# Kernel optimization log

Hardware: AMD Instinct MI355X
Metric: run time of the kernel (lower is better)

## Reference

```python
import jax, jax.numpy as jnp
import numpy as np

B, T, N, E = 4, 32, 370, 11840
H, HEADS, DH, L, K = 64, 4, 16, 3, 5

def gelu(x):
    return jax.nn.gelu(x, approximate=False)  # torch default GELU is exact erf

def setup_inputs() -> dict:
    key = jax.random.key(0)
    ks = jax.random.split(key, 18)
    s = 0.05  # keep activations well-scaled
    return {
        "x": jax.random.normal(ks[0], (B, T, N, H), jnp.float32),
        "edge_index": jax.random.randint(ks[1], (2, E), 0, N, dtype=jnp.int32),
        "edge_weight": jax.random.uniform(ks[2], (E,), jnp.float32),
        "W_gcn": jax.random.normal(ks[3], (L, H, H), jnp.float32) * s,
        "b_gcn": jax.random.normal(ks[4], (L, H), jnp.float32) * s,
        "W_gat": jax.random.normal(ks[5], (L, H, HEADS * DH), jnp.float32) * s,
        "att_src": jax.random.normal(ks[6], (L, HEADS, DH), jnp.float32) * s,
        "att_dst": jax.random.normal(ks[7], (L, HEADS, DH), jnp.float32) * s,
        "b_gat": jax.random.normal(ks[8], (L, HEADS * DH), jnp.float32) * s,
        "W_t": jax.random.normal(ks[9], (L, H, H, K), jnp.float32) * s,  # (O,I,K)
        "b_t": jax.random.normal(ks[10], (L, H), jnp.float32) * s,
        "ln_g": jnp.ones((L, H), jnp.float32),
        "ln_b": jnp.zeros((L, H), jnp.float32),
        "W1": jax.random.normal(ks[11], (N * H, 256), jnp.float32) * s,
        "b1": jax.random.normal(ks[12], (256,), jnp.float32) * s,
        "W2": jax.random.normal(ks[13], (256, 64), jnp.float32) * s,
        "b2": jax.random.normal(ks[14], (64,), jnp.float32) * s,
    }

def reference(x, edge_index, edge_weight, W_gcn, b_gcn, W_gat, att_src, att_dst,
              b_gat, W_t, b_t, ln_g, ln_b, W1, b1, W2, b2):
    Bb, Tt, Nn, Ff = x.shape
    G = Bb * Tt
    nL = W_gcn.shape[0]
    heads, dh = att_src.shape[1], att_src.shape[2]
    Hh = heads * dh
    # shared topology across all G graphs; add self-loops (PyG default, fill=1.0)
    src, dst = edge_index[0], edge_index[1]
    loop = jnp.arange(Nn, dtype=src.dtype)
    src2 = jnp.concatenate([src, loop])
    dst2 = jnp.concatenate([dst, loop])
    ew2 = jnp.concatenate([edge_weight, jnp.ones((Nn,), edge_weight.dtype)])
    # symmetric GCN normalization (same for every graph in the batch)
    deg = jnp.zeros((Nn,), x.dtype).at[dst2].add(ew2)
    dis = jnp.where(deg > 0, jax.lax.rsqrt(deg), jnp.zeros_like(deg))
    gnorm = dis[src2] * ew2 * dis[dst2]                       # (E2,)
    h = x.reshape(G, Nn, Ff)
    for l in range(nL):
        # ---- GCNConv: transform -> gather -> weighted scatter-add ----
        hw = h @ W_gcn[l]                                     # (G,N,H)
        msg = hw[:, src2] * gnorm[None, :, None]              # (G,E2,H)
        g = jnp.zeros_like(hw).at[:, dst2].add(msg) + b_gcn[l]
        g = gelu(g)
        # ---- GATConv: per-edge softmax attention over incoming edges ----
        gh = (g @ W_gat[l]).reshape(G, Nn, heads, dh)
        asrc = (gh * att_src[l]).sum(-1)                      # (G,N,heads)
        adst = (gh * att_dst[l]).sum(-1)
        e = jax.nn.leaky_relu(asrc[:, src2] + adst[:, dst2], negative_slope=0.2)
        m = jnp.full((G, Nn, heads), -jnp.inf, e.dtype).at[:, dst2].max(e)
        ex = jnp.exp(e - m[:, dst2])
        den = jnp.zeros((G, Nn, heads), e.dtype).at[:, dst2].add(ex)
        alpha = ex / den[:, dst2]                             # (G,E2,heads)
        msgs = gh[:, src2] * alpha[..., None]                 # (G,E2,heads,dh)
        out = jnp.zeros_like(gh).at[:, dst2].add(msgs).reshape(G, Nn, Hh) + b_gat[l]
        # ---- residual + LayerNorm ----
        r = out + h[..., :Hh]
        mu = r.mean(-1, keepdims=True)
        var = ((r - mu) ** 2).mean(-1, keepdims=True)
        h = (r - mu) * jax.lax.rsqrt(var + 1e-5) * ln_g[l] + ln_b[l]
    # ---- temporal convs over T per (batch, node) ----
    Hc = h.shape[-1]
    xt = h.reshape(Bb, Tt, Nn, Hc).transpose(0, 2, 3, 1).reshape(Bb * Nn, Hc, Tt)
    for l in range(nL):
        c = jax.lax.conv_general_dilated(
            xt, W_t[l], (1,), "SAME", dimension_numbers=("NCH", "OIH", "NCH"))
        xt = gelu(c + b_t[l][None, :, None]) + xt
    z = xt.reshape(Bb, Nn, Hc, Tt).transpose(0, 3, 1, 2).reshape(Bb, Tt, Nn * Hc)
    return gelu(z @ W1 + b1) @ W2 + b2
```

## Files before the change

kernel.cpp:

```cpp
#include <hip/hip_runtime.h>
#include <hip/hip_bf16.h>

#define B_   4
#define T_   32
#define N_   370
#define NP_  384
#define E_   11840
#define E2_  12210
#define H_   64
#define G_   128
#define GN_  47360
#define BN_  1480
#define NH_  23680
#define ECAP 320
#define KCH_ 128
#define NCH_ 185

typedef __hip_bfloat16 bf;
typedef short short8 __attribute__((ext_vector_type(8)));
typedef float f32x4 __attribute__((ext_vector_type(4)));

__device__ __forceinline__ float gelu_f(float x){
  return 0.5f * x * (1.0f + erff(x * 0.7071067811865475f));
}
__device__ __forceinline__ float lrelu(float v){ return v > 0.f ? v : 0.2f * v; }
__device__ __forceinline__ float b2f(bf x){ return __bfloat162float(x); }
__device__ __forceinline__ void store_bf4(bf* p, float4 v){
  bf tmp[4] = {__float2bfloat16(v.x), __float2bfloat16(v.y),
               __float2bfloat16(v.z), __float2bfloat16(v.w)};
  *(ushort4*)p = *(const ushort4*)tmp;
}
__device__ __forceinline__ void load_bf8(const bf* p, float* v){
  uint4 u = *(const uint4*)p;
  unsigned ua[4] = {u.x, u.y, u.z, u.w};
  #pragma unroll
  for (int i = 0; i < 4; ++i){
    v[2*i]   = __uint_as_float(ua[i] << 16);
    v[2*i+1] = __uint_as_float(ua[i] & 0xffff0000u);
  }
}

__global__ __launch_bounds__(1024) void k_degscan(const int* __restrict__ ei,
    const float* __restrict__ ew, float* __restrict__ degG,
    int* __restrict__ offs, int* __restrict__ cursor){
  __shared__ float degS[512];
  __shared__ int cntS[512];
  int tid = threadIdx.x;
  if (tid < 512){ degS[tid] = 0.f; cntS[tid] = 0; }
  __syncthreads();
  for (int e = tid; e < E2_; e += 1024){
    int dst = (e < E_) ? ei[E_ + e] : (e - E_);
    float w = (e < E_) ? ew[e] : 1.0f;
    atomicAdd(&degS[dst], w);
    atomicAdd(&cntS[dst], 1);
  }
  __syncthreads();
  if (tid < N_) degG[tid] = degS[tid];
  if (tid < 64){
    int lane = tid;
    int run = 0;
    for (int c0 = 0; c0 < N_; c0 += 64){
      int n = c0 + lane;
      int v = (n < N_) ? cntS[n] : 0;
      int s = v;
      #pragma unroll
      for (int m = 1; m < 64; m <<= 1){
        int t = __shfl_up(s, m, 64);
        if (lane >= m) s += t;
      }
      int excl = run + s - v;
      if (n < N_){ offs[n] = excl; cursor[n] = excl; }
      run += __shfl(s, 63, 64);
    }
    if (lane == 0) offs[N_] = run;
  }
}

__global__ void k_gfa(const int* __restrict__ ei, const float* __restrict__ ew,
                      const float* __restrict__ deg, int* __restrict__ cursor,
                      int* __restrict__ csr_soff, float* __restrict__ A32){
  int e = blockIdx.x * 256 + threadIdx.x;
  if (e >= E2_) return;
  int s = (e < E_) ? ei[e] : (e - E_);
  int d = (e < E_) ? ei[E_ + e] : (e - E_);
  float w = (e < E_) ? ew[e] : 1.0f;
  float ds = deg[s] > 0.f ? rsqrtf(deg[s]) : 0.f;
  float dd = deg[d] > 0.f ? rsqrtf(deg[d]) : 0.f;
  float gn = ds * w * dd;
  int pos = atomicAdd(&cursor[d], 1);
  csr_soff[pos] = s << 13;
  atomicAdd(&A32[d * NP_ + s], gn);
}

__global__ void k_prep(const float* __restrict__ A32, bf* __restrict__ A16,
                       const float* __restrict__ W_gcn, const float* __restrict__ W_gat,
                       bf* __restrict__ WT, const float* __restrict__ Wt,
                       bf* __restrict__ WB){
  int b = blockIdx.x;
  if (b < 144){
    int i = b * 256 + threadIdx.x;
    float4 v = *(const float4*)&A32[i * 4];
    store_bf4(&A16[i * 4], v);
  } else if (b < 240){
    int i = (b - 144) * 256 + threadIdx.x;
    int ci = i & 63;
    int co = (i >> 6) & 63;
    int m  = (i >> 12) & 1;
    int l  = i >> 13;
    const float* W = m ? W_gat : W_gcn;
    WT[i] = __float2bfloat16(W[(size_t)(l * 64 + ci) * 64 + co]);
  } else {
    int i = (b - 240) * 256 + threadIdx.x;
    int j = i & 7;
    int r = i >> 3;
    int lane = r & 63;
    int mi = (r >> 6) & 3;
    int t2 = r >> 8;
    int kk = t2 % 10, l = t2 / 10;
    int ho = mi * 16 + (lane & 15);
    int k  = kk >> 1;
    int ci = (kk & 1) * 32 + (lane >> 4) * 8 + j;
    WB[i] = __float2bfloat16(Wt[((l * 64 + ho) * 64 + ci) * 5 + k]);
  }
}

__global__ __launch_bounds__(256) void k_ht(const float* __restrict__ hin,
                                            bf* __restrict__ h16T){
  __shared__ float ts[64 * 68];
  int g = blockIdx.x, nt = blockIdx.y;
  int n0 = nt * 64;
  int tid = threadIdx.x;
  {
    int u = tid & 15, r = tid >> 4;
    #pragma unroll
    for (int it = 0; it < 4; ++it){
      int nr = it * 16 + r;
      int n = n0 + nr;
      float4 v = (n < N_) ? *(const float4*)&hin[((size_t)g * N_ + n) * 64 + u * 4]
                          : make_float4(0.f, 0.f, 0.f, 0.f);
      ts[(u * 4 + 0) * 68 + nr] = v.x;
      ts[(u * 4 + 1) * 68 + nr] = v.y;
      ts[(u * 4 + 2) * 68 + nr] = v.z;
      ts[(u * 4 + 3) * 68 + nr] = v.w;
    }
  }
  __syncthreads();
  {
    int u = tid & 7, c = tid >> 3;
    #pragma unroll
    for (int it = 0; it < 2; ++it){
      int cc = it * 32 + c;
      float4 a0 = *(const float4*)&ts[cc * 68 + u * 8];
      float4 a1 = *(const float4*)&ts[cc * 68 + u * 8 + 4];
      bf bvs[8] = {__float2bfloat16(a0.x), __float2bfloat16(a0.y),
                   __float2bfloat16(a0.z), __float2bfloat16(a0.w),
                   __float2bfloat16(a1.x), __float2bfloat16(a1.y),
                   __float2bfloat16(a1.z), __float2bfloat16(a1.w)};
      *(uint4*)&h16T[((size_t)g * 64 + cc) * NP_ + n0 + u * 8] = *(const uint4*)bvs;
    }
  }
}

__global__ __launch_bounds__(256) void k_gcn_dense(const bf* __restrict__ h16T,
    const bf* __restrict__ A16, const bf* __restrict__ WT,
    const float* __restrict__ b_gcn, const float* __restrict__ att_s,
    const float* __restrict__ att_d, bf* __restrict__ gh16,
    float* __restrict__ asrc, float* __restrict__ adst){
  __shared__ bf As[64 * 136];
  __shared__ bf Bs[64 * 136];
  __shared__ bf Ws1[64 * 72];
  __shared__ bf Ws2[64 * 72];
  __shared__ bf ts[64 * 72];
  int tid = threadIdx.x;
  int g = blockIdx.x;
  int m0 = blockIdx.y * 64;
  {
    int u = tid & 7, r0w = tid >> 3;
    #pragma unroll
    for (int it = 0; it < 2; ++it){
      int r = r0w + it * 32;
      *(uint4*)&Ws1[r * 72 + u * 8] = *(const uint4*)&WT[(size_t)r * 64 + u * 8];
      *(uint4*)&Ws2[r * 72 + u * 8] = *(const uint4*)&WT[(size_t)(64 + r) * 64 + u * 8];
    }
  }
  int lane = tid & 63, w = tid >> 6;
  int lr = lane & 15, lg = lane >> 4;
  f32x4 acc[4];
  #pragma unroll
  for (int nt = 0; nt < 4; ++nt){ f32x4 zv = {0.f,0.f,0.f,0.f}; acc[nt] = zv; }
  for (int kc = 0; kc < 3; ++kc){
    int u = tid & 15, r = tid >> 4;
    #pragma unroll
    for (int it = 0; it < 4; ++it){
      int row = it * 16 + r;
      *(uint4*)&As[row * 136 + u * 8] =
          *(const uint4*)&A16[(size_t)(m0 + row) * NP_ + kc * 128 + u * 8];
      *(uint4*)&Bs[row * 136 + u * 8] =
          *(const uint4*)&h16T[((size_t)g * 64 + row) * NP_ + kc * 128 + u * 8];
    }
    __syncthreads();
    #pragma unroll
    for (int ks = 0; ks < 4; ++ks){
      short8 af = *(const short8*)&As[(w * 16 + lr) * 136 + ks * 32 + lg * 8];
      #pragma unroll
      for (int nt = 0; nt < 4; ++nt){
        short8 bfr = *(const short8*)&Bs[(nt * 16 + lr) * 136 + ks * 32 + lg * 8];
        acc[nt] = __builtin_amdgcn_mfma_f32_16x16x32_bf16(af, bfr, acc[nt], 0, 0, 0);
      }
    }
    __syncthreads();
  }
  #pragma unroll
  for (int nt = 0; nt < 4; ++nt)
    #pragma unroll
    for (int q = 0; q < 4; ++q)
      ts[(w * 16 + lg * 4 + q) * 72 + nt * 16 + lr] = __float2bfloat16(acc[nt][q]);
  f32x4 acc2[4];
  #pragma unroll
  for (int nt = 0; nt < 4; ++nt){ f32x4 zv = {0.f,0.f,0.f,0.f}; acc2[nt] = zv; }
  #pragma unroll
  for (int ks = 0; ks < 2; ++ks){
    short8 af = *(const short8*)&ts[(w * 16 + lr) * 72 + ks * 32 + lg * 8];
    #pragma unroll
    for (int nt = 0; nt < 4; ++nt){
      short8 bfr = *(const short8*)&Ws1[(nt * 16 + lr) * 72 + ks * 32 + lg * 8];
      acc2[nt] = __builtin_amdgcn_mfma_f32_16x16x32_bf16(af, bfr, acc2[nt], 0, 0, 0);
    }
  }
  #pragma unroll
  for (int nt = 0; nt < 4; ++nt){
    float bv = b_gcn[nt * 16 + lr];
    #pragma unroll
    for (int q = 0; q < 4; ++q){
      float gv = gelu_f(acc2[nt][q] + bv);
      ts[(w * 16 + lg * 4 + q) * 72 + nt * 16 + lr] = __float2bfloat16(gv);
    }
  }
  f32x4 acc3[4];
  #pragma unroll
  for (int nt = 0; nt < 4; ++nt){ f32x4 zv = {0.f,0.f,0.f,0.f}; acc3[nt] = zv; }
  #pragma unroll
  for (int ks = 0; ks < 2; ++ks){
    short8 af = *(const short8*)&ts[(w * 16 + lr) * 72 + ks * 32 + lg * 8];
    #pragma unroll
    for (int nt = 0; nt < 4; ++nt){
      short8 bfr = *(const short8*)&Ws2[(nt * 16 + lr) * 72 + ks * 32 + lg * 8];
      acc3[nt] = __builtin_amdgcn_mfma_f32_16x16x32_bf16(af, bfr, acc3[nt], 0, 0, 0);
    }
  }
  #pragma unroll
  for (int nt = 0; nt < 4; ++nt){
    float sa = att_s[nt * 16 + lr];
    float sd = att_d[nt * 16 + lr];
    float ps[4], pd[4];
    #pragma unroll
    for (int q = 0; q < 4; ++q){
      int n = m0 + w * 16 + lg * 4 + q;
      if (n < N_)
        gh16[((size_t)n * G_ + g) * 64 + nt * 16 + lr] = __float2bfloat16(acc3[nt][q]);
      ps[q] = acc3[nt][q] * sa;
      pd[q] = acc3[nt][q] * sd;
    }
    #pragma unroll
    for (int q = 0; q < 4; ++q){
      ps[q] += __shfl_xor(ps[q], 1, 64); ps[q] += __shfl_xor(ps[q], 2, 64);
      ps[q] += __shfl_xor(ps[q], 4, 64); ps[q] += __shfl_xor(ps[q], 8, 64);
      pd[q] += __shfl_xor(pd[q], 1, 64); pd[q] += __shfl_xor(pd[q], 2, 64);
      pd[q] += __shfl_xor(pd[q], 4, 64); pd[q] += __shfl_xor(pd[q], 8, 64);
    }
    if (lr == 0){
      #pragma unroll
      for (int q = 0; q < 4; ++q){
        int n = m0 + w * 16 + lg * 4 + q;
        if (n < N_){
          asrc[((size_t)n * G_ + g) * 4 + nt] = ps[q];
          adst[((size_t)n * G_ + g) * 4 + nt] = pd[q];
        }
      }
    }
  }
}

__global__ __launch_bounds__(256) void k_gat_agg(const bf* __restrict__ gh,
    const float* __restrict__ asrc, const float* __restrict__ adst,
    const int* __restrict__ csr_soff, const int* __restrict__ offs,
    const float* __restrict__ b_gat, const float* __restrict__ ln_g,
    const float* __restrict__ ln_b, const float* __restrict__ hin,
    float* __restrict__ hout){
  __shared__ int sS[ECAP];
  int nb = blockIdx.x;
  int n = nb % N_;
  int gg = nb / N_;
  int tid = threadIdx.x;
  int o0 = offs[n], o1 = offs[n + 1];
  int deg = o1 - o0;
  int cap = deg < ECAP ? deg : ECAP;
  for (int i = tid; i < cap; i += 256) sS[i] = csr_soff[o0 + i];
  __syncthreads();
  int ql = tid >> 3, c8 = tid & 7;
  int g = gg * 32 + ql;
  int head = c8 >> 1;
  int gh4 = g * 4 + head;
  int toff = gg * 2048 + ql * 64 + c8 * 8;
  float adv = adst[n * 512 + gh4];
  float den = 0.f;
  float a[8];
  #pragma unroll
  for (int j = 0; j < 8; ++j) a[j] = 0.f;
  int p = 0;
  for (; p + 2 <= cap; p += 2){
    int s0 = sS[p], s1 = sS[p+1];
    float w0 = __expf(lrelu(asrc[(s0 >> 4) + gh4] + adv));
    float w1 = __expf(lrelu(asrc[(s1 >> 4) + gh4] + adv));
    den += w0 + w1;
    float v0[8], v1[8];
    load_bf8(gh + s0 + toff, v0);
    load_bf8(gh + s1 + toff, v1);
    #pragma unroll
    for (int j = 0; j < 8; ++j) a[j] += w0 * v0[j] + w1 * v1[j];
  }
  for (; p < cap; ++p){
    int sv = sS[p];
    float w0 = __expf(lrelu(asrc[(sv >> 4) + gh4] + adv));
    den += w0;
    float v[8];
    load_bf8(gh + sv + toff, v);
    #pragma unroll
    for (int j = 0; j < 8; ++j) a[j] += w0 * v[j];
  }
  for (int r = cap; r < deg; ++r){
    int sv = csr_soff[o0 + r];
    float w0 = __expf(lrelu(asrc[(sv >> 4) + gh4] + adv));
    den += w0;
    float v[8];
    load_bf8(gh + sv + toff, v);
    #pragma unroll
    for (int j = 0; j < 8; ++j) a[j] += w0 * v[j];
  }
  float inv = 1.f / den;
  float4 bg0 = *(const float4*)&b_gat[c8 * 8];
  float4 bg1 = *(const float4*)&b_gat[c8 * 8 + 4];
  float bb[8] = {bg0.x, bg0.y, bg0.z, bg0.w, bg1.x, bg1.y, bg1.z, bg1.w};
  size_t hbase = ((size_t)g * N_ + n) * 64 + c8 * 8;
  float4 h0 = *(const float4*)&hin[hbase];
  float4 h1 = *(const float4*)&hin[hbase + 4];
  float hh[8] = {h0.x, h0.y, h0.z, h0.w, h1.x, h1.y, h1.z, h1.w};
  float r8[8];
  float s1 = 0.f;
  #pragma unroll
  for (int j = 0; j < 8; ++j){
    r8[j] = a[j] * inv + bb[j] + hh[j];
    s1 += r8[j];
  }
  s1 += __shfl_xor(s1, 1, 64); s1 += __shfl_xor(s1, 2, 64); s1 += __shfl_xor(s1, 4, 64);
  float mu = s1 * (1.f / 64.f);
  float s2 = 0.f;
  #pragma unroll
  for (int j = 0; j < 8; ++j){
    float d = r8[j] - mu;
    s2 += d * d;
  }
  s2 += __shfl_xor(s2, 1, 64); s2 += __shfl_xor(s2, 2, 64); s2 += __shfl_xor(s2, 4, 64);
  float rstd = rsqrtf(s2 * (1.f / 64.f) + 1e-5f);
  float4 lg0 = *(const float4*)&ln_g[c8 * 8];
  float4 lg1 = *(const float4*)&ln_g[c8 * 8 + 4];
  float4 lb0 = *(const float4*)&ln_b[c8 * 8];
  float4 lb1 = *(const float4*)&ln_b[c8 * 8 + 4];
  float lg[8] = {lg0.x, lg0.y, lg0.z, lg0.w, lg1.x, lg1.y, lg1.z, lg1.w};
  float lb[8] = {lb0.x, lb0.y, lb0.z, lb0.w, lb1.x, lb1.y, lb1.z, lb1.w};
  float4 w0v, w1v;
  w0v.x = (r8[0]-mu)*rstd*lg[0]+lb[0]; w0v.y = (r8[1]-mu)*rstd*lg[1]+lb[1];
  w0v.z = (r8[2]-mu)*rstd*lg[2]+lb[2]; w0v.w = (r8[3]-mu)*rstd*lg[3]+lb[3];
  w1v.x = (r8[4]-mu)*rstd*lg[4]+lb[4]; w1v.y = (r8[5]-mu)*rstd*lg[5]+lb[5];
  w1v.z = (r8[6]-mu)*rstd*lg[6]+lb[6]; w1v.w = (r8[7]-mu)*rstd*lg[7]+lb[7];
  *(float4*)&hout[hbase] = w0v;
  *(float4*)&hout[hbase + 4] = w1v;
}

__global__ __launch_bounds__(256) void k_wt_tfuse(const float* __restrict__ h,
    const bf* __restrict__ WB, const float* __restrict__ bt,
    bf* __restrict__ z16, const float* __restrict__ W1, bf* __restrict__ W1T){
  __shared__ __align__(16) char smem[17408];
  int tid = threadIdx.x;
  if (blockIdx.x >= BN_){
    float* ts = (float*)smem;
    int bi = blockIdx.x - BN_;
    int k0 = (bi % 370) * 64, c0 = (bi / 370) * 64;
    #pragma unroll
    for (int it = 0; it < 4; ++it){
      int idx = it * 256 + tid;
      int r = idx >> 4, c4 = (idx & 15) * 4;
      *(float4*)&ts[r * 68 + c4] = *(const float4*)&W1[(size_t)(k0 + r) * 256 + c0 + c4];
    }
    __syncthreads();
    #pragma unroll
    for (int it = 0; it < 4; ++it){
      int idx = it * 256 + tid;
      int c = idx >> 4, k4 = (idx & 15) * 4;
      float4 v;
      v.x = ts[(k4 + 0) * 68 + c];
      v.y = ts[(k4 + 1) * 68 + c];
      v.z = ts[(k4 + 2) * 68 + c];
      v.w = ts[(k4 + 3) * 68 + c];
      store_bf4(&W1T[(size_t)(c0 + c) * 23680 + k0 + k4], v);
    }
    return;
  }
  float* xf = (float*)smem;
  char* xTg = smem + 8704;
  int w = tid >> 6, lane = tid & 63;
  int bn = blockIdx.x;
  int b = bn / N_, n = bn - b * N_;
  int lq = lane >> 4, lr = lane & 15;
  #pragma unroll
  for (int r = 0; r < 2; ++r){
    int t = w * 8 + r * 4 + lq;
    int c4 = lr * 4;
    float4 v = *(const float4*)&h[((size_t)(b * T_ + t) * N_ + n) * 64 + c4];
    *(float4*)&xf[t * 68 + c4] = v;
    int row = t + 2;
    bf bv[4] = {__float2bfloat16(v.x), __float2bfloat16(v.y),
                __float2bfloat16(v.z), __float2bfloat16(v.w)};
    int bo = (c4 * 2) ^ ((row & 7) << 4);
    *(uint2*)&xTg[row * 128 + bo] = *(const uint2*)bv;
  }
  if (w == 0){
    int zr = (lq < 2) ? lq : (lq + 32);
    *(uint2*)&xTg[zr * 128 + lr * 8] = make_uint2(0u, 0u);
  }
  __syncthreads();
  for (int l = 0; l < 3; ++l){
    const short8* Wp = (const short8*)(WB + (size_t)l * 20480);
    f32x4 acc[2];
    {
      f32x4 zv = {0.f, 0.f, 0.f, 0.f};
      acc[0] = zv; acc[1] = zv;
    }
    #pragma unroll 2
    for (int kk = 0; kk < 10; ++kk){
      int k = kk >> 1;
      int bbyte = (kk & 1) * 64 + lq * 16;
      short8 bfr[2];
      #pragma unroll
      for (int nj = 0; nj < 2; ++nj){
        int row = nj * 16 + lr + k;
        bfr[nj] = *(const short8*)&xTg[row * 128 + (bbyte ^ ((row & 7) << 4))];
      }
      short8 afr = Wp[(kk * 4 + w) * 64 + lane];
      #pragma unroll
      for (int nj = 0; nj < 2; ++nj)
        acc[nj] = __builtin_amdgcn_mfma_f32_16x16x32_bf16(
            afr, bfr[nj], acc[nj], 0, 0, 0);
    }
    __syncthreads();
    {
      int ho0 = w * 16 + lq * 4;
      float4 bt4 = *(const float4*)&bt[l * 64 + ho0];
      float btv[4] = {bt4.x, bt4.y, bt4.z, bt4.w};
      #pragma unroll
      for (int nj = 0; nj < 2; ++nj){
        int t = nj * 16 + lr;
        float4 xr = *(const float4*)&xf[t * 68 + ho0];
        float xv[4] = {xr.x, xr.y, xr.z, xr.w};
        float ov[4];
        #pragma unroll
        for (int q = 0; q < 4; ++q)
          ov[q] = gelu_f(acc[nj][q] + btv[q]) + xv[q];
        *(float4*)&xf[t * 68 + ho0] = make_float4(ov[0], ov[1], ov[2], ov[3]);
        int row = t + 2;
        bf bvv[4] = {__float2bfloat16(ov[0]), __float2bfloat16(ov[1]),
                     __float2bfloat16(ov[2]), __float2bfloat16(ov[3])};
        *(uint2*)&xTg[row * 128 + ((ho0 * 2) ^ ((row & 7) << 4))] = *(const uint2*)bvv;
      }
    }
    __syncthreads();
  }
  #pragma unroll
  for (int r = 0; r < 2; ++r){
    int t = w * 8 + r * 4 + lq;
    int c4 = lr * 4;
    float4 v = *(const float4*)&xf[t * 68 + c4];
    store_bf4(&z16[(size_t)(b * T_ + t) * NH_ + n * 64 + c4], v);
  }
}

__global__ __launch_bounds__(256) void k_mlp1(const bf* __restrict__ z16,
    const bf* __restrict__ W1T, float* __restrict__ pbuf){
  __shared__ bf zs[128 * 136];
  __shared__ bf ws[128 * 136];
  int kc = blockIdx.x;
  int ch = blockIdx.y;
  int tid = threadIdx.x;
  int k0 = kc * KCH_;
  {
    int u = tid & 15, r = tid >> 4;
    #pragma unroll
    for (int it = 0; it < 8; ++it){
      int row = it * 16 + r;
      uint4 v = *(const uint4*)&z16[(size_t)row * NH_ + k0 + u * 8];
      *(uint4*)&zs[row * 136 + u * 8] = v;
    }
    #pragma unroll
    for (int it = 0; it < 8; ++it){
      int col = it * 16 + r;
      uint4 v = *(const uint4*)&W1T[(size_t)(ch * 128 + col) * 23680 + k0 + u * 8];
      *(uint4*)&ws[col * 136 + u * 8] = v;
    }
  }
  __syncthreads();
  int lane = tid & 63, w = tid >> 6;
  int lr = lane & 15, lg = lane >> 4;
  int wr = w * 32;
  f32x4 acc[2][8];
  #pragma unroll
  for (int mt = 0; mt < 2; ++mt)
    #pragma unroll
    for (int nt = 0; nt < 8; ++nt){
      f32x4 zv = {0.f, 0.f, 0.f, 0.f};
      acc[mt][nt] = zv;
    }
  #pragma unroll
  for (int ks = 0; ks < 4; ++ks){
    short8 af[2], bfr[8];
    #pragma unroll
    for (int mt = 0; mt < 2; ++mt)
      af[mt] = *(const short8*)&zs[(wr + mt * 16 + lr) * 136 + ks * 32 + lg * 8];
    #pragma unroll
    for (int nt = 0; nt < 8; ++nt)
      bfr[nt] = *(const short8*)&ws[(nt * 16 + lr) * 136 + ks * 32 + lg * 8];
    #pragma unroll
    for (int mt = 0; mt < 2; ++mt)
      #pragma unroll
      for (int nt = 0; nt < 8; ++nt)
        acc[mt][nt] = __builtin_amdgcn_mfma_f32_16x16x32_bf16(
            af[mt], bfr[nt], acc[mt][nt], 0, 0, 0);
  }
  float* pb = pbuf + (size_t)kc * 32768 + ch * 128;
  #pragma unroll
  for (int mt = 0; mt < 2; ++mt)
    #pragma unroll
    for (int nt = 0; nt < 8; ++nt){
      int row = wr + mt * 16 + lg * 4;
      int col = nt * 16 + lr;
      #pragma unroll
      for (int q = 0; q < 4; ++q)
        pb[(size_t)(row + q) * 256 + col] = acc[mt][nt][q];
    }
}

__global__ __launch_bounds__(64) void k_mlp2(const float* __restrict__ pbuf,
    const float* __restrict__ b1, const float* __restrict__ W2,
    const float* __restrict__ b2, float* __restrict__ outp){
  __shared__ float a[256];
  int row = blockIdx.x, tid = threadIdx.x;
  const float* p = pbuf + (size_t)row * 256 + tid * 4;
  float sx = 0.f, sy = 0.f, sz = 0.f, sw = 0.f;
  #pragma unroll 5
  for (int kc = 0; kc < NCH_; ++kc){
    float4 v = *(const float4*)&p[(size_t)kc * 32768];
    sx += v.x; sy += v.y; sz += v.z; sw += v.w;
  }
  float4 bv = *(const float4*)&b1[tid * 4];
  a[tid * 4 + 0] = gelu_f(sx + bv.x);
  a[tid * 4 + 1] = gelu_f(sy + bv.y);
  a[tid * 4 + 2] = gelu_f(sz + bv.z);
  a[tid * 4 + 3] = gelu_f(sw + bv.w);
  __syncthreads();
  float acc = b2[tid];
  for (int i = 0; i < 256; ++i) acc += a[i] * W2[i * 64 + tid];
  outp[row * 64 + tid] = acc;
}

extern "C" void kernel_launch(void* const* d_in, const int* in_sizes, int n_in,
                              void* d_out, int out_size, void* d_ws, size_t ws_size,
                              hipStream_t stream){
  const float* x     = (const float*)d_in[0];
  const int*   ei    = (const int*)  d_in[1];
  const float* ew    = (const float*)d_in[2];
  const float* W_gcn = (const float*)d_in[3];
  const float* b_gcn = (const float*)d_in[4];
  const float* W_gat = (const float*)d_in[5];
  const float* att_s = (const float*)d_in[6];
  const float* att_d = (const float*)d_in[7];
  const float* b_gat = (const float*)d_in[8];
  const float* W_t   = (const float*)d_in[9];
  const float* b_t   = (const float*)d_in[10];
  const float* ln_g  = (const float*)d_in[11];
  const float* ln_b  = (const float*)d_in[12];
  const float* W1    = (const float*)d_in[13];
  const float* b1    = (const float*)d_in[14];
  const float* W2    = (const float*)d_in[15];
  const float* b2    = (const float*)d_in[16];
  float* outp = (float*)d_out;

  float* F = (float*)d_ws;
  size_t off = 0;
  float* asrc   = F + off; off += 189440;
  float* adst   = F + off; off += 189440;
  float* WTf    = F + off; off += 61440;
  float* h      = F + off; off += 3031040;
  float* bufB   = F + off; off += 3031040;
  float* bufC   = F + off; off += 3031040;
  float* bufD   = F + off; off += 3031040;
  float* pbuf   = F + off; off += (size_t)NCH_ * 32768;
  int* I        = (int*)(F + off);
  int* offs     = I;
  int* cursor   = I + 512;
  int* csr_soff = I + 1024;

  bf* WB     = (bf*)WTf;
  bf* WTT    = (bf*)(WTf + 30720);
  bf* h16T   = (bf*)bufB;
  bf* W1T    = (bf*)bufB;
  float* A32 = bufC;
  float* degG= bufC + 147456;
  bf* A16    = (bf*)(bufC + 148480);
  bf* gh16   = (bf*)bufD;
  bf* z16    = (bf*)bufD;

  hipMemsetAsync(A32, 0, (size_t)NP_ * NP_ * sizeof(float), stream);

  k_degscan<<<1, 1024, 0, stream>>>(ei, ew, degG, offs, cursor);
  k_gfa<<<48, 256, 0, stream>>>(ei, ew, degG, cursor, csr_soff, A32);
  k_prep<<<480, 256, 0, stream>>>(A32, A16, W_gcn, W_gat, WTT, W_t, WB);

  dim3 gdn(G_, 6);
  for (int l = 0; l < 3; ++l){
    const float* hin = (l == 0) ? x : h;
    k_ht<<<gdn, 256, 0, stream>>>(hin, h16T);
    k_gcn_dense<<<gdn, 256, 0, stream>>>(h16T, A16, WTT + (size_t)l * 8192,
                                         b_gcn + l * 64, att_s + l * 64, att_d + l * 64,
                                         gh16, asrc, adst);
    k_gat_agg<<<1480, 256, 0, stream>>>(gh16, asrc, adst, csr_soff, offs,
                                        b_gat + l * 64, ln_g + l * 64, ln_b + l * 64,
                                        hin, h);
  }

  k_wt_tfuse<<<2 * BN_, 256, 0, stream>>>(h, WB, b_t, z16, W1, W1T);

  dim3 g1(NCH_, 2);
  k_mlp1<<<g1, 256, 0, stream>>>(z16, W1T, pbuf);
  k_mlp2<<<128, 64, 0, stream>>>(pbuf, b1, W2, b2, outp);
}
```

Measured before the change: 311.7 us.

## Fuse transpose into GCN GEMM, merge graph-setup kernels, remap blocks per XCD

Removes the separate k_ht transpose/convert kernel by loading fp32 node features directly inside k_gcn_dense and packing them as bf16 pairs into the transposed shared tile. Merges degree scan and CSR/adjacency build into one single-block kernel using shared-memory degrees and cursors. Remaps block indices in k_gcn_dense and k_gat_agg so blocks sharing a graph or node land on the same XCD for better L2 locality. It trades a kernel launch and an intermediate buffer round-trip for uncoalesced-ish strided LDS writes and a serialized single-block edge build.

```diff
diff --git a/kernel.cpp b/kernel.cpp
--- a/kernel.cpp
+++ b/kernel.cpp
@@ -30,6 +30,10 @@
                __float2bfloat16(v.z), __float2bfloat16(v.w)};
   *(ushort4*)p = *(const ushort4*)tmp;
 }
+__device__ __forceinline__ unsigned pk_bf2(float a, float b){
+  bf lo = __float2bfloat16(a), hi = __float2bfloat16(b);
+  return (unsigned)*(unsigned short*)&lo | ((unsigned)*(unsigned short*)&hi << 16);
+}
 __device__ __forceinline__ void load_bf8(const bf* p, float* v){
   uint4 u = *(const uint4*)p;
   unsigned ua[4] = {u.x, u.y, u.z, u.w};
@@ -40,11 +44,12 @@
   }
 }
 
-__global__ __launch_bounds__(1024) void k_degscan(const int* __restrict__ ei,
-    const float* __restrict__ ew, float* __restrict__ degG,
-    int* __restrict__ offs, int* __restrict__ cursor){
+__global__ __launch_bounds__(1024) void k_degscan_gfa(const int* __restrict__ ei,
+    const float* __restrict__ ew, int* __restrict__ offs,
+    int* __restrict__ csr_soff, float* __restrict__ A32){
   __shared__ float degS[512];
   __shared__ int cntS[512];
+  __shared__ int curS[512];
   int tid = threadIdx.x;
   if (tid < 512){ degS[tid] = 0.f; cntS[tid] = 0; }
   __syncthreads();
@@ -55,7 +60,6 @@
     atomicAdd(&cntS[dst], 1);
   }
   __syncthreads();
-  if (tid < N_) degG[tid] = degS[tid];
   if (tid < 64){
     int lane = tid;
     int run = 0;
@@ -69,27 +73,22 @@
         if (lane >= m) s += t;
       }
       int excl = run + s - v;
-      if (n < N_){ offs[n] = excl; cursor[n] = excl; }
+      if (n < N_){ offs[n] = excl; curS[n] = excl; }
       run += __shfl(s, 63, 64);
     }
     if (lane == 0) offs[N_] = run;
   }
-}
-
-__global__ void k_gfa(const int* __restrict__ ei, const float* __restrict__ ew,
-                      const float* __restrict__ deg, int* __restrict__ cursor,
-                      int* __restrict__ csr_soff, float* __restrict__ A32){
-  int e = blockIdx.x * 256 + threadIdx.x;
-  if (e >= E2_) return;
-  int s = (e < E_) ? ei[e] : (e - E_);
-  int d = (e < E_) ? ei[E_ + e] : (e - E_);
-  float w = (e < E_) ? ew[e] : 1.0f;
-  float ds = deg[s] > 0.f ? rsqrtf(deg[s]) : 0.f;
-  float dd = deg[d] > 0.f ? rsqrtf(deg[d]) : 0.f;
-  float gn = ds * w * dd;
-  int pos = atomicAdd(&cursor[d], 1);
-  csr_soff[pos] = s << 13;
-  atomicAdd(&A32[d * NP_ + s], gn);
+  __syncthreads();
+  for (int e = tid; e < E2_; e += 1024){
+    int s = (e < E_) ? ei[e] : (e - E_);
+    int d = (e < E_) ? ei[E_ + e] : (e - E_);
+    float w = (e < E_) ? ew[e] : 1.0f;
+    float ds = degS[s] > 0.f ? rsqrtf(degS[s]) : 0.f;
+    float dd = degS[d] > 0.f ? rsqrtf(degS[d]) : 0.f;
+    int pos = atomicAdd(&curS[d], 1);
+    csr_soff[pos] = s << 13;
+    atomicAdd(&A32[d * NP_ + s], ds * w * dd);
+  }
 }
 
 __global__ void k_prep(const float* __restrict__ A32, bf* __restrict__ A16,
@@ -124,44 +123,7 @@
   }
 }
 
-__global__ __launch_bounds__(256) void k_ht(const float* __restrict__ hin,
-                                            bf* __restrict__ h16T){
-  __shared__ float ts[64 * 68];
-  int g = blockIdx.x, nt = blockIdx.y;
-  int n0 = nt * 64;
-  int tid = threadIdx.x;
-  {
-    int u = tid & 15, r = tid >> 4;
-    #pragma unroll
-    for (int it = 0; it < 4; ++it){
-      int nr = it * 16 + r;
-      int n = n0 + nr;
-      float4 v = (n < N_) ? *(const float4*)&hin[((size_t)g * N_ + n) * 64 + u * 4]
-                          : make_float4(0.f, 0.f, 0.f, 0.f);
-      ts[(u * 4 + 0) * 68 + nr] = v.x;
-      ts[(u * 4 + 1) * 68 + nr] = v.y;
-      ts[(u * 4 + 2) * 68 + nr] = v.z;
-      ts[(u * 4 + 3) * 68 + nr] = v.w;
-    }
-  }
-  __syncthreads();
-  {
-    int u = tid & 7, c = tid >> 3;
-    #pragma unroll
-    for (int it = 0; it < 2; ++it){
-      int cc = it * 32 + c;
-      float4 a0 = *(const float4*)&ts[cc * 68 + u * 8];
-      float4 a1 = *(const float4*)&ts[cc * 68 + u * 8 + 4];
-      bf bvs[8] = {__float2bfloat16(a0.x), __float2bfloat16(a0.y),
-                   __float2bfloat16(a0.z), __float2bfloat16(a0.w),
-                   __float2bfloat16(a1.x), __float2bfloat16(a1.y),
-                   __float2bfloat16(a1.z), __float2bfloat16(a1.w)};
-      *(uint4*)&h16T[((size_t)g * 64 + cc) * NP_ + n0 + u * 8] = *(const uint4*)bvs;
-    }
-  }
-}
-
-__global__ __launch_bounds__(256) void k_gcn_dense(const bf* __restrict__ h16T,
+__global__ __launch_bounds__(256) void k_gcn_dense(const float* __restrict__ hin,
     const bf* __restrict__ A16, const bf* __restrict__ WT,
     const float* __restrict__ b_gcn, const float* __restrict__ att_s,
     const float* __restrict__ att_d, bf* __restrict__ gh16,
@@ -172,8 +134,10 @@
   __shared__ bf Ws2[64 * 72];
   __shared__ bf ts[64 * 72];
   int tid = threadIdx.x;
-  int g = blockIdx.x;
-  int m0 = blockIdx.y * 64;
+  int b0 = blockIdx.x;
+  int xcd = b0 & 7, jj6 = b0 >> 3;
+  int g = xcd * 16 + jj6 / 6;
+  int m0 = (jj6 % 6) * 64;
   {
     int u = tid & 7, r0w = tid >> 3;
     #pragma unroll
@@ -195,8 +159,20 @@
       int row = it * 16 + r;
       *(uint4*)&As[row * 136 + u * 8] =
           *(const uint4*)&A16[(size_t)(m0 + row) * NP_ + kc * 128 + u * 8];
-      *(uint4*)&Bs[row * 136 + u * 8] =
-          *(const uint4*)&h16T[((size_t)g * 64 + row) * NP_ + kc * 128 + u * 8];
+    }
+    #pragma unroll
+    for (int it = 0; it < 4; ++it){
+      int nn = (it * 16 + r) * 2;
+      int n = kc * 128 + nn;
+      float4 v0 = (n < N_) ? *(const float4*)&hin[((size_t)g * N_ + n) * 64 + u * 4]
+                           : make_float4(0.f, 0.f, 0.f, 0.f);
+      float4 v1 = (n + 1 < N_) ? *(const float4*)&hin[((size_t)g * N_ + n + 1) * 64 + u * 4]
+                               : make_float4(0.f, 0.f, 0.f, 0.f);
+      float a0[4] = {v0.x, v0.y, v0.z, v0.w};
+      float a1[4] = {v1.x, v1.y, v1.z, v1.w};
+      #pragma unroll
+      for (int q = 0; q < 4; ++q)
+        *(unsigned*)&Bs[(u * 4 + q) * 136 + nn] = pk_bf2(a0[q], a1[q]);
     }
     __syncthreads();
     #pragma unroll
@@ -288,9 +264,9 @@
     const float* __restrict__ ln_b, const float* __restrict__ hin,
     float* __restrict__ hout){
   __shared__ int sS[ECAP];
-  int nb = blockIdx.x;
-  int n = nb % N_;
-  int gg = nb / N_;
+  int b0 = blockIdx.x;
+  int gg = (b0 & 7) >> 1;
+  int n = (b0 >> 3) * 2 + (b0 & 1);
   int tid = threadIdx.x;
   int o0 = offs[n], o1 = offs[n + 1];
   int deg = o1 - o0;
@@ -605,30 +581,24 @@
   float* pbuf   = F + off; off += (size_t)NCH_ * 32768;
   int* I        = (int*)(F + off);
   int* offs     = I;
-  int* cursor   = I + 512;
-  int* csr_soff = I + 1024;
+  int* csr_soff = I + 512;
 
   bf* WB     = (bf*)WTf;
   bf* WTT    = (bf*)(WTf + 30720);
-  bf* h16T   = (bf*)bufB;
   bf* W1T    = (bf*)bufB;
   float* A32 = bufC;
-  float* degG= bufC + 147456;
-  bf* A16    = (bf*)(bufC + 148480);
+  bf* A16    = (bf*)(bufC + 147456);
   bf* gh16   = (bf*)bufD;
   bf* z16    = (bf*)bufD;
 
   hipMemsetAsync(A32, 0, (size_t)NP_ * NP_ * sizeof(float), stream);
 
-  k_degscan<<<1, 1024, 0, stream>>>(ei, ew, degG, offs, cursor);
-  k_gfa<<<48, 256, 0, stream>>>(ei, ew, degG, cursor, csr_soff, A32);
+  k_degscan_gfa<<<1, 1024, 0, stream>>>(ei, ew, offs, csr_soff, A32);
   k_prep<<<480, 256, 0, stream>>>(A32, A16, W_gcn, W_gat, WTT, W_t, WB);
 
-  dim3 gdn(G_, 6);
   for (int l = 0; l < 3; ++l){
     const float* hin = (l == 0) ? x : h;
-    k_ht<<<gdn, 256, 0, stream>>>(hin, h16T);
-    k_gcn_dense<<<gdn, 256, 0, stream>>>(h16T, A16, WTT + (size_t)l * 8192,
+    k_gcn_dense<<<768, 256, 0, stream>>>(hin, A16, WTT + (size_t)l * 8192,
                                          b_gcn + l * 64, att_s + l * 64, att_d + l * 64,
                                          gh16, asrc, adst);
     k_gat_agg<<<1480, 256, 0, stream>>>(gh16, asrc, adst, csr_soff, offs,
```

Measured after the change: 340.1 us. 1.09x slower.
